# Kernel optimization log

Measured on AMD Instinct MI355X. Metric: run time of the kernel, lower is better.

Reference implementation:

```python
import jax, jax.numpy as jnp
import numpy as np

N_NODES = 100000
N_EDGES = 3200000
N_GRAPHS = 1024


def _glorot(key, shape):
    fan_in, fan_out = shape[0], shape[1]
    lim = (6.0 / (fan_in + fan_out)) ** 0.5
    return jax.random.uniform(key, shape, jnp.float32, -lim, lim)


def setup_inputs() -> dict:
    key = jax.random.key(0)
    ks = jax.random.split(key, 12)
    x = jax.random.normal(ks[0], (N_NODES, 2), jnp.float32)
    edge_attr = jax.random.normal(ks[1], (N_EDGES, 1), jnp.float32)
    edge_index = jax.random.randint(ks[2], (2, N_EDGES), 0, N_NODES, jnp.int64)
    batch = jnp.sort(jax.random.randint(ks[3], (N_NODES,), 0, N_GRAPHS, jnp.int64))
    params = {
        'w_node': _glorot(ks[4], (2, 32)),   'b_node': jnp.zeros((32,), jnp.float32),
        'w_edge': _glorot(ks[5], (1, 32)),   'b_edge': jnp.zeros((32,), jnp.float32),
        'w1': _glorot(ks[6], (32, 64)),      'b1': jnp.zeros((64,), jnp.float32),
        'w2': _glorot(ks[7], (64, 64)),      'b2': jnp.zeros((64,), jnp.float32),
        'wf1': _glorot(ks[8], (64, 32)),     'bf1': jnp.zeros((32,), jnp.float32),
        'wf2': _glorot(ks[9], (32, 1)),      'bf2': jnp.zeros((1,), jnp.float32),
    }
    return {'x': x, 'edge_attr': edge_attr, 'edge_index': edge_index, 'batch': batch, **params}


def gcn_conv(x, edge_index, w, b):
    # PyG GCNConv: out = D^{-1/2} (A + I) D^{-1/2} (x @ w) + b
    n = x.shape[0]
    xw = x @ w  # [N, F_out]
    loops = jnp.arange(n, dtype=edge_index.dtype)
    src = jnp.concatenate([edge_index[0], loops])  # messages flow src -> dst
    dst = jnp.concatenate([edge_index[1], loops])
    deg = jax.ops.segment_sum(jnp.ones_like(dst, dtype=xw.dtype), dst, num_segments=n)
    dis = jnp.where(deg > 0, jax.lax.rsqrt(jnp.maximum(deg, 1e-12)), 0.0)
    norm = dis[src] * dis[dst]  # [E+N]
    msgs = xw[src] * norm[:, None]  # gather + scale, [E+N, F_out]
    out = jax.ops.segment_sum(msgs, dst, num_segments=n)
    return out + b


def reference(x, edge_attr, edge_index, batch,
              w_node, b_node, w_edge, b_edge,
              w1, b1, w2, b2, wf1, bf1, wf2, bf2):
    h = jax.nn.relu(x @ w_node + b_node)               # [N, 32]
    e = jax.nn.relu(edge_attr @ w_edge + b_edge)       # [E, 32] (computed, unused downstream as in source)
    h = jax.nn.relu(gcn_conv(h, edge_index, w1, b1))   # [N, 64]
    h = jax.nn.relu(gcn_conv(h, edge_index, w2, b2))   # [N, 64]
    # global mean pool over graphs
    sums = jax.ops.segment_sum(h, batch, num_segments=N_GRAPHS)  # [G, 64]
    cnts = jax.ops.segment_sum(jnp.ones((h.shape[0],), h.dtype), batch, num_segments=N_GRAPHS)
    pooled = sums / jnp.maximum(cnts, 1.0)[:, None]
    g = jax.nn.relu(pooled @ wf1 + bf1)                # [G, 32]
    out = g @ wf2 + bf2                                # [G, 1]
    return out
```

## Files before the change

### kernel.cpp

```cpp
#include <hip/hip_runtime.h>


#define NBMAX 512
#define BCAP 12288
#define CAPL 10240

__global__ void k_initcur(int* __restrict__ bcur) {
    bcur[threadIdx.x] = threadIdx.x * BCAP;
}

__global__ void k_passA(const int* __restrict__ ei, int* __restrict__ bcur,
                        unsigned int* __restrict__ pairBuf, int E) {
    __shared__ int h[NBMAX];
    __shared__ int base[NBMAX];
    const int T = 256, EPT = 32;
    int chunk = blockIdx.x * (T * EPT);
    int t = threadIdx.x;
    h[t] = 0; h[t + 256] = 0;
    __syncthreads();
    int nE = min(E - chunk, T * EPT);
    for (int i = t; i < nE; i += T)
        atomicAdd(&h[ei[E + chunk + i] >> 8], 1);
    __syncthreads();
    for (int bb = t; bb < NBMAX; bb += T) {
        int c = h[bb];
        base[bb] = c > 0 ? atomicAdd(&bcur[bb], c) : 0;
        h[bb] = 0;
    }
    __syncthreads();
    for (int i = t; i < nE; i += T) {
        int s = ei[chunk + i];
        int d = ei[E + chunk + i];
        int bb = d >> 8;
        int pos = base[bb] + atomicAdd(&h[bb], 1);
        pairBuf[pos] = ((unsigned int)(d & 255) << 24) | (unsigned int)s;
    }
}

__global__ void k_bucketScan(const int* __restrict__ bcur, int* __restrict__ bucketBase,
                             int* __restrict__ rowPtr, int N, int E, int NB) {
    __shared__ int sh[NBMAX];
    int t = threadIdx.x;
    int c = (t < NB) ? (bcur[t] - t * BCAP) : 0;
    sh[t] = c;
    __syncthreads();
    for (int off = 1; off < NBMAX; off <<= 1) {
        int v = (t >= off) ? sh[t - off] : 0;
        __syncthreads();
        sh[t] += v;
        __syncthreads();
    }
    bucketBase[t] = sh[t] - c;
    if (t == 0) rowPtr[N] = E;
}

__global__ void k_passB(const int* __restrict__ bcur, const int* __restrict__ bucketBase,
                        const unsigned int* __restrict__ pairBuf, int* __restrict__ rowPtr,
                        float* __restrict__ dis, int* __restrict__ srcIdx, int N) {
    __shared__ unsigned int eLds[CAPL];
    __shared__ int hist[256];
    __shared__ int scan[256];
    int b = blockIdx.x;
    int t = threadIdx.x;
    int count = bcur[b] - b * BCAP;
    int gbase = bucketBase[b];
    const unsigned int* src = pairBuf + (size_t)b * BCAP;
    hist[t] = 0;
    int nStage = min(count, CAPL);
    for (int i = t; i < nStage; i += 256) eLds[i] = src[i];
    __syncthreads();
    for (int i = t; i < nStage; i += 256) atomicAdd(&hist[eLds[i] >> 24], 1);
    for (int i = CAPL + t; i < count; i += 256) atomicAdd(&hist[src[i] >> 24], 1);
    __syncthreads();
    int c = hist[t];
    scan[t] = c;
    __syncthreads();
    for (int off = 1; off < 256; off <<= 1) {
        int v = (t >= off) ? scan[t - off] : 0;
        __syncthreads();
        scan[t] += v;
        __syncthreads();
    }
    int excl = scan[t] - c;
    int node = (b << 8) + t;
    if (node < N) {
        rowPtr[node] = gbase + excl;
        dis[node] = rsqrtf((float)c + 1.0f);
    }
    hist[t] = excl;
    __syncthreads();
    for (int i = t; i < nStage; i += 256) {
        unsigned int e = eLds[i];
        int pos = atomicAdd(&hist[e >> 24], 1);
        srcIdx[gbase + pos] = (int)(e & 0xFFFFFFu);
    }
    for (int i = CAPL + t; i < count; i += 256) {
        unsigned int e = src[i];
        int pos = atomicAdd(&hist[e >> 24], 1);
        srcIdx[gbase + pos] = (int)(e & 0xFFFFFFu);
    }
}

__global__ void k_node_init(const float* __restrict__ x, const float* __restrict__ w,
                            const float* __restrict__ b, const float* __restrict__ dis,
                            float* __restrict__ h0, int N) {
    int tid = blockIdx.x * blockDim.x + threadIdx.x;
    if (tid >= N * 32) return;
    int n = tid >> 5, f = tid & 31;
    float v = x[2 * n] * w[f] + x[2 * n + 1] * w[32 + f] + b[f];
    v = v > 0.f ? v : 0.f;
    h0[tid] = v * dis[n];
}

__global__ void k_agg64(const int* __restrict__ rowPtr, const int* __restrict__ srcIdx,
                        const float* __restrict__ y, const float* __restrict__ dis,
                        float* __restrict__ z, int N) {
    constexpr int QF = 16, RPI = 4, U = 8, CH = RPI * U;
    int wid = (blockIdx.x * blockDim.x + threadIdx.x) >> 6;
    if (wid >= N) return;
    int lane = threadIdx.x & 63;
    int q = lane & (QF - 1);
    int r = lane / QF;
    int beg = rowPtr[wid], end = rowPtr[wid + 1];
    const float4* yq = (const float4*)y;
    float4 acc = {0.f, 0.f, 0.f, 0.f};
    if (r == 0) acc = yq[(size_t)wid * QF + q];
    if (end > beg) {
        int last = end - 1;
        for (int base = beg; base < end; base += CH) {
            int s[U];
            float m[U];
#pragma unroll
            for (int u = 0; u < U; ++u) {
                int i = base + r + u * RPI;
                m[u] = (i < end) ? 1.f : 0.f;
                s[u] = srcIdx[min(i, last)];
            }
#pragma unroll
            for (int u = 0; u < U; ++u) {
                float4 a = yq[(size_t)s[u] * QF + q];
                acc.x = fmaf(a.x, m[u], acc.x);
                acc.y = fmaf(a.y, m[u], acc.y);
                acc.z = fmaf(a.z, m[u], acc.z);
                acc.w = fmaf(a.w, m[u], acc.w);
            }
        }
    }
#pragma unroll
    for (int mk = QF; mk < 64; mk <<= 1) {
        acc.x += __shfl_xor(acc.x, mk);
        acc.y += __shfl_xor(acc.y, mk);
        acc.z += __shfl_xor(acc.z, mk);
        acc.w += __shfl_xor(acc.w, mk);
    }
    if (r == 0) {
        float dv = dis[wid];
        float4 o = {acc.x * dv, acc.y * dv, acc.z * dv, acc.w * dv};
        ((float4*)z)[(size_t)wid * QF + q] = o;
    }
}

__global__ void k_agg32mm(const int* __restrict__ rowPtr, const int* __restrict__ srcIdx,
                          const float* __restrict__ y, const float* __restrict__ dis,
                          const float* __restrict__ w1, const float* __restrict__ b1,
                          float* __restrict__ hOut, int N) {
    constexpr int QF = 8, RPI = 8, U = 4, CH = RPI * U;
    int wid = (blockIdx.x * blockDim.x + threadIdx.x) >> 6;
    if (wid >= N) return;
    int lane = threadIdx.x & 63;
    int q = lane & (QF - 1);
    int r = lane / QF;
    int beg = rowPtr[wid], end = rowPtr[wid + 1];
    const float4* yq = (const float4*)y;
    float4 acc = {0.f, 0.f, 0.f, 0.f};
    if (r == 0) acc = yq[(size_t)wid * QF + q];
    if (end > beg) {
        int last = end - 1;
        for (int base = beg; base < end; base += CH) {
            int s[U];
            float m[U];
#pragma unroll
            for (int u = 0; u < U; ++u) {
                int i = base + r + u * RPI;
                m[u] = (i < end) ? 1.f : 0.f;
                s[u] = srcIdx[min(i, last)];
            }
#pragma unroll
            for (int u = 0; u < U; ++u) {
                float4 a = yq[(size_t)s[u] * QF + q];
                acc.x = fmaf(a.x, m[u], acc.x);
                acc.y = fmaf(a.y, m[u], acc.y);
                acc.z = fmaf(a.z, m[u], acc.z);
                acc.w = fmaf(a.w, m[u], acc.w);
            }
        }
    }
#pragma unroll
    for (int mk = QF; mk < 64; mk <<= 1) {
        acc.x += __shfl_xor(acc.x, mk);
        acc.y += __shfl_xor(acc.y, mk);
        acc.z += __shfl_xor(acc.z, mk);
        acc.w += __shfl_xor(acc.w, mk);
    }
    int f = lane;
    float s = 0.f;
#pragma unroll
    for (int q2 = 0; q2 < QF; ++q2) {
        float bx = __shfl(acc.x, q2);
        float by = __shfl(acc.y, q2);
        float bz = __shfl(acc.z, q2);
        float bw = __shfl(acc.w, q2);
        s = fmaf(bx, w1[(4 * q2 + 0) * 64 + f], s);
        s = fmaf(by, w1[(4 * q2 + 1) * 64 + f], s);
        s = fmaf(bz, w1[(4 * q2 + 2) * 64 + f], s);
        s = fmaf(bw, w1[(4 * q2 + 3) * 64 + f], s);
    }
    float dv = dis[wid];
    float h = fmaxf(fmaf(dv, s, b1[f]), 0.f) * dv;
    hOut[(size_t)wid * 64 + f] = h;
}

__global__ void k_poolhead(const float* __restrict__ z2, const float* __restrict__ w2,
                           const float* __restrict__ b2, const int* __restrict__ batch,
                           const float* __restrict__ wf1, const float* __restrict__ bf1,
                           const float* __restrict__ wf2, const float* __restrict__ bf2,
                           float* __restrict__ out, int N) {
    __shared__ float red[4][64];
    __shared__ float pooled[64];
    __shared__ float gv[32];
    __shared__ int range[2];
    int g = blockIdx.x;
    int t = threadIdx.x;
    if (t < 2) {
        int target = g + t;
        int lo = 0, hi = N;
        while (lo < hi) {
            int mid = (lo + hi) >> 1;
            if (batch[mid] < target) lo = mid + 1; else hi = mid;
        }
        range[t] = lo;
    }
    __syncthreads();
    int s = range[0], e = range[1];
    int w = t >> 6, f = t & 63;
    float wcol[64];
#pragma unroll
    for (int k = 0; k < 64; ++k) wcol[k] = w2[k * 64 + f];
    float bf = b2[f];
    float acc = 0.f;
    for (int n = s + w; n < e; n += 4) {
        const float4* zr = (const float4*)(z2 + (size_t)n * 64);
        float h = bf;
#pragma unroll
        for (int kq = 0; kq < 16; ++kq) {
            float4 zv = zr[kq];
            h += zv.x * wcol[4 * kq + 0];
            h += zv.y * wcol[4 * kq + 1];
            h += zv.z * wcol[4 * kq + 2];
            h += zv.w * wcol[4 * kq + 3];
        }
        acc += fmaxf(h, 0.f);
    }
    red[w][f] = acc;
    __syncthreads();
    if (t < 64) {
        float c = (float)(e - s);
        c = c > 1.f ? c : 1.f;
        pooled[t] = (red[0][t] + red[1][t] + red[2][t] + red[3][t]) / c;
    }
    __syncthreads();
    if (t < 32) {
        float sv = bf1[t];
#pragma unroll
        for (int k = 0; k < 64; ++k) sv += pooled[k] * wf1[k * 32 + t];
        gv[t] = fmaxf(sv, 0.f);
    }
    __syncthreads();
    if (t == 0) {
        float sv = bf2[0];
#pragma unroll
        for (int j = 0; j < 32; ++j) sv += gv[j] * wf2[j];
        out[g] = sv;
    }
}

extern "C" void kernel_launch(void* const* d_in, const int* in_sizes, int n_in,
                              void* d_out, int out_size, void* d_ws, size_t ws_size,
                              hipStream_t stream) {
    const float* x      = (const float*)d_in[0];
    const int*   ei     = (const int*)d_in[2];
    const int*   batch  = (const int*)d_in[3];
    const float* w_node = (const float*)d_in[4];
    const float* b_node = (const float*)d_in[5];
    const float* w1  = (const float*)d_in[8];
    const float* b1  = (const float*)d_in[9];
    const float* w2  = (const float*)d_in[10];
    const float* b2  = (const float*)d_in[11];
    const float* wf1 = (const float*)d_in[12];
    const float* bf1 = (const float*)d_in[13];
    const float* wf2 = (const float*)d_in[14];
    const float* bf2 = (const float*)d_in[15];
    float* out = (float*)d_out;

    const int N = in_sizes[0] / 2;
    const int E = in_sizes[2] / 2;
    const int G = out_size;
    const int NB = (N + 255) >> 8;

    auto align256 = [](size_t v) { return (v + 255) & ~(size_t)255; };
    char* ws = (char*)d_ws;
    size_t off = 0;
    float* dis     = (float*)(ws + off); off += align256((size_t)N * 4);
    int*   rowPtr  = (int*)(ws + off);   off += align256((size_t)(N + 1) * 4);
    int*   bcur    = (int*)(ws + off);   off += align256((size_t)NBMAX * 4);
    int*   bbase   = (int*)(ws + off);   off += align256((size_t)NBMAX * 4);
    int*   srcIdx  = (int*)(ws + off);   off += align256((size_t)E * 4);
    float* region1 = (float*)(ws + off); off += align256((size_t)N * 64 * 4);
    float* hT1     = (float*)(ws + off); off += align256((size_t)N * 64 * 4);

    unsigned int* pairBuf = (unsigned int*)region1;
    float* hT0 = region1;
    float* z2  = region1;

    const int B = 256;

    k_initcur<<<1, NBMAX, 0, stream>>>(bcur);
    {
        int nblk = (E + B * 32 - 1) / (B * 32);
        k_passA<<<nblk, B, 0, stream>>>(ei, bcur, pairBuf, E);
    }
    k_bucketScan<<<1, NBMAX, 0, stream>>>(bcur, bbase, rowPtr, N, E, NB);
    k_passB<<<NB, B, 0, stream>>>(bcur, bbase, pairBuf, rowPtr, dis, srcIdx, N);

    k_node_init<<<(N * 32 + B - 1) / B, B, 0, stream>>>(x, w_node, b_node, dis, hT0, N);

    k_agg32mm<<<(N * 64 + B - 1) / B, B, 0, stream>>>(rowPtr, srcIdx, hT0, dis,
                                                      w1, b1, hT1, N);

    k_agg64<<<(N * 64 + B - 1) / B, B, 0, stream>>>(rowPtr, srcIdx, hT1, dis, z2, N);

    k_poolhead<<<G, B, 0, stream>>>(z2, w2, b2, batch, wf1, bf1, wf2, bf2, out, N);
}
```

Before: 303.2 us.

## Fuse bucket scan and node init into passB, add nontemporal memory ops

The separate bucket-scan kernel is removed: each passB block now computes its own global base by reducing the bucket counts of all earlier buckets. The node-init kernel is folded into passB, and hT0 gets its own buffer instead of aliasing the pair buffer. Nontemporal loads and stores are added on streaming edge and index traffic. The pool head now runs 512 threads per block, stages w2 in shared memory instead of per-thread registers, and reduces over 8 partial sums. Together these cut two launches and lower register pressure, at the cost of redundant prefix work in every passB block and extra workspace.

Measured after the change: 475.8 us. +56.9%, slower.

```diff
diff --git a/kernel.cpp b/kernel.cpp
--- a/kernel.cpp
+++ b/kernel.cpp
@@ -1,5 +1,7 @@
 #include <hip/hip_runtime.h>
 
+
+typedef float vfloat4 __attribute__((ext_vector_type(4)));
 
 #define NBMAX 512
 #define BCAP 12288
@@ -33,130 +35,87 @@
         int d = ei[E + chunk + i];
         int bb = d >> 8;
         int pos = base[bb] + atomicAdd(&h[bb], 1);
-        pairBuf[pos] = ((unsigned int)(d & 255) << 24) | (unsigned int)s;
-    }
-}
-
-__global__ void k_bucketScan(const int* __restrict__ bcur, int* __restrict__ bucketBase,
-                             int* __restrict__ rowPtr, int N, int E, int NB) {
-    __shared__ int sh[NBMAX];
-    int t = threadIdx.x;
-    int c = (t < NB) ? (bcur[t] - t * BCAP) : 0;
-    sh[t] = c;
-    __syncthreads();
-    for (int off = 1; off < NBMAX; off <<= 1) {
-        int v = (t >= off) ? sh[t - off] : 0;
-        __syncthreads();
-        sh[t] += v;
-        __syncthreads();
-    }
-    bucketBase[t] = sh[t] - c;
-    if (t == 0) rowPtr[N] = E;
-}
-
-__global__ void k_passB(const int* __restrict__ bcur, const int* __restrict__ bucketBase,
-                        const unsigned int* __restrict__ pairBuf, int* __restrict__ rowPtr,
-                        float* __restrict__ dis, int* __restrict__ srcIdx, int N) {
+        __builtin_nontemporal_store(((unsigned int)(d & 255) << 24) | (unsigned int)s,
+                                    pairBuf + pos);
+    }
+}
+
+__global__ void k_passB(const int* __restrict__ bcur,
+                        const unsigned int* __restrict__ pairBuf,
+                        int* __restrict__ rowPtr, float* __restrict__ dis,
+                        int* __restrict__ srcIdx, const float* __restrict__ x,
+                        const float* __restrict__ wn, const float* __restrict__ bn,
+                        float* __restrict__ h0, int N, int E) {
     __shared__ unsigned int eLds[CAPL];
     __shared__ int hist[256];
     __shared__ int scan[256];
+    __shared__ float disL[256];
+    __shared__ float wsh[64];
+    __shared__ float bsh[32];
     int b = blockIdx.x;
     int t = threadIdx.x;
     int count = bcur[b] - b * BCAP;
-    int gbase = bucketBase[b];
     const unsigned int* src = pairBuf + (size_t)b * BCAP;
+    int part = 0;
+    for (int i = t; i < b; i += 256) part += bcur[i] - i * BCAP;
+    scan[t] = part;
+    __syncthreads();
+    for (int o = 128; o > 0; o >>= 1) {
+        if (t < o) scan[t] += scan[t + o];
+        __syncthreads();
+    }
+    int gbase = scan[0];
+    __syncthreads();
     hist[t] = 0;
+    if (t < 64) wsh[t] = wn[t];
+    if (t < 32) bsh[t] = bn[t];
     int nStage = min(count, CAPL);
-    for (int i = t; i < nStage; i += 256) eLds[i] = src[i];
+    for (int i = t; i < nStage; i += 256) eLds[i] = __builtin_nontemporal_load(src + i);
     __syncthreads();
     for (int i = t; i < nStage; i += 256) atomicAdd(&hist[eLds[i] >> 24], 1);
-    for (int i = CAPL + t; i < count; i += 256) atomicAdd(&hist[src[i] >> 24], 1);
+    for (int i = CAPL + t; i < count; i += 256)
+        atomicAdd(&hist[__builtin_nontemporal_load(src + i) >> 24], 1);
     __syncthreads();
     int c = hist[t];
     scan[t] = c;
     __syncthreads();
-    for (int off = 1; off < 256; off <<= 1) {
-        int v = (t >= off) ? scan[t - off] : 0;
+    for (int o = 1; o < 256; o <<= 1) {
+        int v = (t >= o) ? scan[t - o] : 0;
         __syncthreads();
         scan[t] += v;
         __syncthreads();
     }
     int excl = scan[t] - c;
     int node = (b << 8) + t;
+    float dval = rsqrtf((float)c + 1.0f);
+    disL[t] = dval;
     if (node < N) {
         rowPtr[node] = gbase + excl;
-        dis[node] = rsqrtf((float)c + 1.0f);
+        dis[node] = dval;
+        if (node == N - 1) rowPtr[N] = E;
     }
     hist[t] = excl;
     __syncthreads();
     for (int i = t; i < nStage; i += 256) {
         unsigned int e = eLds[i];
         int pos = atomicAdd(&hist[e >> 24], 1);
-        srcIdx[gbase + pos] = (int)(e & 0xFFFFFFu);
+        __builtin_nontemporal_store((int)(e & 0xFFFFFFu), srcIdx + gbase + pos);
     }
     for (int i = CAPL + t; i < count; i += 256) {
-        unsigned int e = src[i];
+        unsigned int e = __builtin_nontemporal_load(src + i);
         int pos = atomicAdd(&hist[e >> 24], 1);
-        srcIdx[gbase + pos] = (int)(e & 0xFFFFFFu);
-    }
-}
-
-__global__ void k_node_init(const float* __restrict__ x, const float* __restrict__ w,
-                            const float* __restrict__ b, const float* __restrict__ dis,
-                            float* __restrict__ h0, int N) {
-    int tid = blockIdx.x * blockDim.x + threadIdx.x;
-    if (tid >= N * 32) return;
-    int n = tid >> 5, f = tid & 31;
-    float v = x[2 * n] * w[f] + x[2 * n + 1] * w[32 + f] + b[f];
-    v = v > 0.f ? v : 0.f;
-    h0[tid] = v * dis[n];
-}
-
-__global__ void k_agg64(const int* __restrict__ rowPtr, const int* __restrict__ srcIdx,
-                        const float* __restrict__ y, const float* __restrict__ dis,
-                        float* __restrict__ z, int N) {
-    constexpr int QF = 16, RPI = 4, U = 8, CH = RPI * U;
-    int wid = (blockIdx.x * blockDim.x + threadIdx.x) >> 6;
-    if (wid >= N) return;
-    int lane = threadIdx.x & 63;
-    int q = lane & (QF - 1);
-    int r = lane / QF;
-    int beg = rowPtr[wid], end = rowPtr[wid + 1];
-    const float4* yq = (const float4*)y;
-    float4 acc = {0.f, 0.f, 0.f, 0.f};
-    if (r == 0) acc = yq[(size_t)wid * QF + q];
-    if (end > beg) {
-        int last = end - 1;
-        for (int base = beg; base < end; base += CH) {
-            int s[U];
-            float m[U];
-#pragma unroll
-            for (int u = 0; u < U; ++u) {
-                int i = base + r + u * RPI;
-                m[u] = (i < end) ? 1.f : 0.f;
-                s[u] = srcIdx[min(i, last)];
-            }
-#pragma unroll
-            for (int u = 0; u < U; ++u) {
-                float4 a = yq[(size_t)s[u] * QF + q];
-                acc.x = fmaf(a.x, m[u], acc.x);
-                acc.y = fmaf(a.y, m[u], acc.y);
-                acc.z = fmaf(a.z, m[u], acc.z);
-                acc.w = fmaf(a.w, m[u], acc.w);
-            }
-        }
-    }
-#pragma unroll
-    for (int mk = QF; mk < 64; mk <<= 1) {
-        acc.x += __shfl_xor(acc.x, mk);
-        acc.y += __shfl_xor(acc.y, mk);
-        acc.z += __shfl_xor(acc.z, mk);
-        acc.w += __shfl_xor(acc.w, mk);
-    }
-    if (r == 0) {
-        float dv = dis[wid];
-        float4 o = {acc.x * dv, acc.y * dv, acc.z * dv, acc.w * dv};
-        ((float4*)z)[(size_t)wid * QF + q] = o;
+        __builtin_nontemporal_store((int)(e & 0xFFFFFFu), srcIdx + gbase + pos);
+    }
+    __syncthreads();
+    for (int ch = 0; ch < 32; ++ch) {
+        int ln = ch * 8 + (t >> 5);
+        int f = t & 31;
+        int n2 = (b << 8) + ln;
+        if (n2 < N) {
+            float v = x[2 * n2] * wsh[f] + x[2 * n2 + 1] * wsh[32 + f] + bsh[f];
+            v = fmaxf(v, 0.f);
+            h0[(size_t)n2 * 32 + f] = v * disL[ln];
+        }
     }
 }
 
@@ -183,7 +142,7 @@
             for (int u = 0; u < U; ++u) {
                 int i = base + r + u * RPI;
                 m[u] = (i < end) ? 1.f : 0.f;
-                s[u] = srcIdx[min(i, last)];
+                s[u] = __builtin_nontemporal_load(srcIdx + min(i, last));
             }
 #pragma unroll
             for (int u = 0; u < U; ++u) {
@@ -220,17 +179,67 @@
     hOut[(size_t)wid * 64 + f] = h;
 }
 
+__global__ void k_agg64(const int* __restrict__ rowPtr, const int* __restrict__ srcIdx,
+                        const float* __restrict__ y, const float* __restrict__ dis,
+                        float* __restrict__ z, int N) {
+    constexpr int QF = 16, RPI = 4, U = 8, CH = RPI * U;
+    int wid = (blockIdx.x * blockDim.x + threadIdx.x) >> 6;
+    if (wid >= N) return;
+    int lane = threadIdx.x & 63;
+    int q = lane & (QF - 1);
+    int r = lane / QF;
+    int beg = rowPtr[wid], end = rowPtr[wid + 1];
+    const float4* yq = (const float4*)y;
+    float4 acc = {0.f, 0.f, 0.f, 0.f};
+    if (r == 0) acc = yq[(size_t)wid * QF + q];
+    if (end > beg) {
+        int last = end - 1;
+        for (int base = beg; base < end; base += CH) {
+            int s[U];
+            float m[U];
+#pragma unroll
+            for (int u = 0; u < U; ++u) {
+                int i = base + r + u * RPI;
+                m[u] = (i < end) ? 1.f : 0.f;
+                s[u] = __builtin_nontemporal_load(srcIdx + min(i, last));
+            }
+#pragma unroll
+            for (int u = 0; u < U; ++u) {
+                float4 a = yq[(size_t)s[u] * QF + q];
+                acc.x = fmaf(a.x, m[u], acc.x);
+                acc.y = fmaf(a.y, m[u], acc.y);
+                acc.z = fmaf(a.z, m[u], acc.z);
+                acc.w = fmaf(a.w, m[u], acc.w);
+            }
+        }
+    }
+#pragma unroll
+    for (int mk = QF; mk < 64; mk <<= 1) {
+        acc.x += __shfl_xor(acc.x, mk);
+        acc.y += __shfl_xor(acc.y, mk);
+        acc.z += __shfl_xor(acc.z, mk);
+        acc.w += __shfl_xor(acc.w, mk);
+    }
+    if (r == 0) {
+        float dv = dis[wid];
+        vfloat4 o = {acc.x * dv, acc.y * dv, acc.z * dv, acc.w * dv};
+        __builtin_nontemporal_store(o, (vfloat4*)z + (size_t)wid * QF + q);
+    }
+}
+
 __global__ void k_poolhead(const float* __restrict__ z2, const float* __restrict__ w2,
                            const float* __restrict__ b2, const int* __restrict__ batch,
                            const float* __restrict__ wf1, const float* __restrict__ bf1,
                            const float* __restrict__ wf2, const float* __restrict__ bf2,
                            float* __restrict__ out, int N) {
-    __shared__ float red[4][64];
+    __shared__ float w2s[64 * 64];
+    __shared__ float red[8][64];
     __shared__ float pooled[64];
     __shared__ float gv[32];
     __shared__ int range[2];
     int g = blockIdx.x;
     int t = threadIdx.x;
+    for (int i = t; i < 4096; i += 512) w2s[i] = w2[i];
     if (t < 2) {
         int target = g + t;
         int lo = 0, hi = N;
@@ -243,21 +252,18 @@
     __syncthreads();
     int s = range[0], e = range[1];
     int w = t >> 6, f = t & 63;
-    float wcol[64];
-#pragma unroll
-    for (int k = 0; k < 64; ++k) wcol[k] = w2[k * 64 + f];
     float bf = b2[f];
     float acc = 0.f;
-    for (int n = s + w; n < e; n += 4) {
-        const float4* zr = (const float4*)(z2 + (size_t)n * 64);
+    for (int n = s + w; n < e; n += 8) {
+        const vfloat4* zr = (const vfloat4*)(z2 + (size_t)n * 64);
         float h = bf;
 #pragma unroll
         for (int kq = 0; kq < 16; ++kq) {
-            float4 zv = zr[kq];
-            h += zv.x * wcol[4 * kq + 0];
-            h += zv.y * wcol[4 * kq + 1];
-            h += zv.z * wcol[4 * kq + 2];
-            h += zv.w * wcol[4 * kq + 3];
+            vfloat4 zv = __builtin_nontemporal_load(zr + kq);
+            h += zv[0] * w2s[(4 * kq + 0) * 64 + f];
+            h += zv[1] * w2s[(4 * kq + 1) * 64 + f];
+            h += zv[2] * w2s[(4 * kq + 2) * 64 + f];
+            h += zv[3] * w2s[(4 * kq + 3) * 64 + f];
         }
         acc += fmaxf(h, 0.f);
     }
@@ -266,7 +272,10 @@
     if (t < 64) {
         float c = (float)(e - s);
         c = c > 1.f ? c : 1.f;
-        pooled[t] = (red[0][t] + red[1][t] + red[2][t] + red[3][t]) / c;
+        float sum = 0.f;
+#pragma unroll
+        for (int j = 0; j < 8; ++j) sum += red[j][t];
+        pooled[t] = sum / c;
     }
     __syncthreads();
     if (t < 32) {
@@ -313,14 +322,13 @@
     float* dis     = (float*)(ws + off); off += align256((size_t)N * 4);
     int*   rowPtr  = (int*)(ws + off);   off += align256((size_t)(N + 1) * 4);
     int*   bcur    = (int*)(ws + off);   off += align256((size_t)NBMAX * 4);
-    int*   bbase   = (int*)(ws + off);   off += align256((size_t)NBMAX * 4);
     int*   srcIdx  = (int*)(ws + off);   off += align256((size_t)E * 4);
     float* region1 = (float*)(ws + off); off += align256((size_t)N * 64 * 4);
     float* hT1     = (float*)(ws + off); off += align256((size_t)N * 64 * 4);
+    float* hT0     = (float*)(ws + off); off += align256((size_t)N * 32 * 4);
 
     unsigned int* pairBuf = (unsigned int*)region1;
-    float* hT0 = region1;
-    float* z2  = region1;
+    float* z2 = region1;
 
     const int B = 256;
 
@@ -329,15 +337,13 @@
         int nblk = (E + B * 32 - 1) / (B * 32);
         k_passA<<<nblk, B, 0, stream>>>(ei, bcur, pairBuf, E);
     }
-    k_bucketScan<<<1, NBMAX, 0, stream>>>(bcur, bbase, rowPtr, N, E, NB);
-    k_passB<<<NB, B, 0, stream>>>(bcur, bbase, pairBuf, rowPtr, dis, srcIdx, N);
-
-    k_node_init<<<(N * 32 + B - 1) / B, B, 0, stream>>>(x, w_node, b_node, dis, hT0, N);
+    k_passB<<<NB, B, 0, stream>>>(bcur, pairBuf, rowPtr, dis, srcIdx,
+                                  x, w_node, b_node, hT0, N, E);
 
     k_agg32mm<<<(N * 64 + B - 1) / B, B, 0, stream>>>(rowPtr, srcIdx, hT0, dis,
                                                       w1, b1, hT1, N);
 
     k_agg64<<<(N * 64 + B - 1) / B, B, 0, stream>>>(rowPtr, srcIdx, hT1, dis, z2, N);
 
-    k_poolhead<<<G, B, 0, stream>>>(z2, w2, b2, batch, wf1, bf1, wf2, bf2, out, N);
-}
+    k_poolhead<<<G, 512, 0, stream>>>(z2, w2, b2, batch, wf1, bf1, wf2, bf2, out, N);
+}
```
